# Optimization experiments

Hardware: AMD Instinct MI355X
Metric: run time of the kernel (lower is better)

Reference implementation:

```python
import jax, jax.numpy as jnp
import numpy as np

N_HEAD = 16
N_KV = 4
HEAD_DIM = 128
ROPE_BASE = 10000.0
YARN_ORIG = 2048
YARN_TARGET = 8192
YARN_ALPHA = 1.0
YARN_BETA = 1.0
SOFTCAP = 50.0


def _yarn_freqs(seq_len, start=0):
    # inv_freq with YaRN scaling: stretch by (target/orig)**alpha, magnitude 1/beta
    inv_freq = 1.0 / (ROPE_BASE ** (jnp.arange(0, HEAD_DIM, 2, dtype=jnp.float32) / HEAD_DIM))
    scale = (YARN_TARGET / YARN_ORIG) ** YARN_ALPHA
    inv_freq = inv_freq / scale * (1.0 / max(YARN_BETA, 1e-6))
    pos = jnp.arange(start, start + seq_len, dtype=jnp.float32)
    return pos[:, None] * inv_freq[None, :]  # [T, D/2]


def _apply_rope(x, freqs):
    # x: [B, H, T, D], interleaved even/odd rotation
    x_even = x[..., ::2]
    x_odd = x[..., 1::2]
    cos = jnp.cos(freqs)[None, None]  # [1,1,T,D/2]
    sin = jnp.sin(freqs)[None, None]
    y_even = x_even * cos - x_odd * sin
    y_odd = x_odd * cos + x_even * sin
    y = jnp.stack([y_even, y_odd], axis=-1).reshape(x.shape)
    return y


def setup_inputs() -> dict:
    key = jax.random.key(0)
    k1, k2, k3 = jax.random.split(key, 3)
    B, T, C = 2, 2048, 2048
    qkv_dim = (N_HEAD + 2 * N_KV) * HEAD_DIM  # 3072
    x = jax.random.normal(k1, (B, T, C), dtype=jnp.float32)
    w_qkv = jax.random.normal(k2, (C, qkv_dim), dtype=jnp.float32) * (1.0 / np.sqrt(C))
    w_o = jax.random.normal(k3, (C, C), dtype=jnp.float32) * (1.0 / np.sqrt(C))
    return {"x": x, "w_qkv": w_qkv, "w_o": w_o}


def reference(x, w_qkv, w_o):
    B, T, C = x.shape
    qkv = x @ w_qkv  # [B, T, (H+2*Hkv)*D]
    q_dim = N_HEAD * HEAD_DIM
    kv_dim = N_KV * HEAD_DIM
    q = qkv[..., :q_dim].reshape(B, T, N_HEAD, HEAD_DIM).transpose(0, 2, 1, 3)
    k = qkv[..., q_dim:q_dim + kv_dim].reshape(B, T, N_KV, HEAD_DIM).transpose(0, 2, 1, 3)
    v = qkv[..., q_dim + kv_dim:].reshape(B, T, N_KV, HEAD_DIM).transpose(0, 2, 1, 3)

    freqs = _yarn_freqs(T)
    q = _apply_rope(q, freqs)
    k = _apply_rope(k, freqs)

    # GQA: expand kv heads to query heads
    rep = N_HEAD // N_KV
    k = jnp.repeat(k, rep, axis=1)
    v = jnp.repeat(v, rep, axis=1)

    scores = jnp.einsum('bhqd,bhkd->bhqk', q, k) / jnp.sqrt(jnp.float32(HEAD_DIM))
    scores = SOFTCAP * jnp.tanh(scores / SOFTCAP)
    causal = jnp.tril(jnp.ones((T, T), dtype=bool))
    scores = jnp.where(causal[None, None], scores, jnp.float32(-1e9))
    attn = jax.nn.softmax(scores.astype(jnp.float32), axis=-1).astype(q.dtype)
    out = jnp.einsum('bhqk,bhkd->bhqd', attn, v)
    out = out.transpose(0, 2, 1, 3).reshape(B, T, C)
    return out @ w_o
```

## Files before the change

kernel.cpp:

```cpp
#include <hip/hip_runtime.h>
#include <hip/hip_bf16.h>

typedef __attribute__((ext_vector_type(8))) __bf16 bf16x8;
typedef __attribute__((ext_vector_type(2))) __bf16 bf16x2;
typedef __attribute__((ext_vector_type(4))) float f32x4;

#define T_SEQ 2048
#define C_DIM 2048
#define QKV_DIM 3072
#define NKV 4
#define HD 128

#define AS1 __attribute__((address_space(1)))
#define AS3 __attribute__((address_space(3)))

__device__ __forceinline__ unsigned short f2bf(float x) {
    __hip_bfloat16 h = __float2bfloat16(x);
    return __builtin_bit_cast(unsigned short, h);
}
__device__ __forceinline__ float bf2f(unsigned short u) {
    unsigned int i = ((unsigned int)u) << 16;
    return __builtin_bit_cast(float, i);
}
__device__ __forceinline__ unsigned int pkbf(float lo, float hi) {
#if __has_builtin(__builtin_amdgcn_cvt_pk_bf16_f32)
    bf16x2 r = __builtin_amdgcn_cvt_pk_bf16_f32(lo, hi);
    return __builtin_bit_cast(unsigned int, r);
#else
    return ((unsigned int)f2bf(hi) << 16) | (unsigned int)f2bf(lo);
#endif
}
__device__ __forceinline__ f32x4 mfma16(bf16x8 a, bf16x8 b, f32x4 c) {
    return __builtin_amdgcn_mfma_f32_16x16x32_bf16(a, b, c, 0, 0, 0);
}
__device__ __forceinline__ void gload_lds16(const void* g, void* l) {
    __builtin_amdgcn_global_load_lds((const AS1 unsigned int*)g,
                                     (AS3 unsigned int*)l, 16, 0, 0);
}
__device__ __forceinline__ float softcap_exp(float s) {
    const float CX2 = 3.125e-6f;
    const float CT  = 0.12752334197529714f;
    float x2 = s * s * CX2;
    float poly = fmaf(x2, fmaf(x2, 0.13333333f, -0.33333333f), 1.0f);
    return exp2f(s * CT * poly);
}

__global__ __launch_bounds__(256) void cast_f32_to_bf16(
        const float* __restrict__ in, unsigned short* __restrict__ out, int n4) {
    int i = blockIdx.x * 256 + threadIdx.x;
    if (i >= n4) return;
    float4 v = ((const float4*)in)[i];
    uint2 o;
    o.x = pkbf(v.x, v.y);
    o.y = pkbf(v.z, v.w);
    ((uint2*)out)[i] = o;
}

__global__ __launch_bounds__(256) void transpose_cast_f32_bf16(
        const float* __restrict__ in, unsigned short* __restrict__ out,
        int rows, int cols) {
    __shared__ float tile[32][33];
    int c0 = blockIdx.x * 32, r0 = blockIdx.y * 32;
    int tx = threadIdx.x, ty = threadIdx.y;
    #pragma unroll
    for (int i = 0; i < 4; i++)
        tile[ty + 8 * i][tx] = in[(size_t)(r0 + ty + 8 * i) * cols + c0 + tx];
    __syncthreads();
    #pragma unroll
    for (int i = 0; i < 4; i++)
        out[(size_t)(c0 + ty + 8 * i) * rows + r0 + tx] = f2bf(tile[tx][ty + 8 * i]);
}

__global__ __launch_bounds__(256) void pack_v(
        const unsigned short* __restrict__ qkv, unsigned short* __restrict__ vpack) {
    __shared__ unsigned short tile[32][33];
    int c0 = blockIdx.x * 32;
    int r0 = blockIdx.y * 32;
    int tx = threadIdx.x, ty = threadIdx.y;
    #pragma unroll
    for (int i = 0; i < 4; i++)
        tile[ty + 8 * i][tx] =
            qkv[(size_t)(r0 + ty + 8 * i) * QKV_DIM + 2560 + c0 + tx];
    __syncthreads();
    #pragma unroll
    for (int i = 0; i < 4; i++) {
        int dcol = c0 + ty + 8 * i;
        int kv = dcol >> 7, d = dcol & 127;
        int r = r0 + tx;
        int b = r >> 11, t = r & (T_SEQ - 1);
        vpack[(size_t)((b * NKV + kv) * 64 + (t >> 5)) * 4096 +
              (d >> 4) * 512 + ((t >> 3) & 3) * 128 + (d & 15) * 8 + (t & 7)] =
            tile[tx][ty + 8 * i];
    }
}

__global__ __launch_bounds__(256) void yarn_tab_kernel(float2* __restrict__ tab) {
    int idx = blockIdx.x * 256 + threadIdx.x;
    int t = idx >> 6, i = idx & 63;
    float inv = 0.25f * exp2f(-(float)i * (13.287712379549449f / 64.0f));
    float ang = (float)t * inv;
    float s, c;
    __sincosf(ang, &s, &c);
    tab[idx] = make_float2(c, s);
}

__global__ __launch_bounds__(256) void rope_kernel(
        unsigned short* __restrict__ qkv, const float2* __restrict__ tab,
        unsigned short* __restrict__ kpack) {
    int row = blockIdx.x;
    int t = row & (T_SEQ - 1);
    int b = row >> 11;
    const float2* tb = tab + t * 64;
    for (int p = threadIdx.x; p < 1280; p += 256) {
        int head = p >> 6, i = p & 63;
        float2 cs = tb[i];
        size_t idx = (size_t)row * QKV_DIM + head * 128 + 2 * i;
        unsigned int u = *(const unsigned int*)(qkv + idx);
        float e = bf2f((unsigned short)(u & 0xffff));
        float o = bf2f((unsigned short)(u >> 16));
        unsigned int res = pkbf(e * cs.x - o * cs.y, o * cs.x + e * cs.y);
        if (head < 16) {
            *(unsigned int*)(qkv + idx) = res;
        } else {
            int kvh = head - 16;
            unsigned short* dst = kpack +
                (size_t)((b * NKV + kvh) * 128 + (t >> 4)) * 2048 +
                (i >> 2) * 128 + (t & 15) * 8 + (i & 3) * 2;
            *(unsigned int*)dst = res;
        }
    }
}

template <int OUT_BF16>
__global__ __launch_bounds__(256) void gemm_bt(
        const unsigned short* __restrict__ A, const unsigned short* __restrict__ Bt,
        void* __restrict__ Cout, int M, int N, int K) {
    __shared__ __align__(16) unsigned short As[128 * 32];
    __shared__ __align__(16) unsigned short Bs[128 * 32];
    int tid = threadIdx.x;
    int nwg = gridDim.x * gridDim.y;
    int lid = blockIdx.y * gridDim.x + blockIdx.x;
    int work = (lid & 7) * (nwg >> 3) + (lid >> 3);
    int m0 = (work % gridDim.y) * 128;
    int n0 = (work / gridDim.y) * 128;
    int wave = tid >> 6, lane = tid & 63;
    int wm = (wave & 1) * 64, wn = (wave >> 1) * 64;
    int l15 = lane & 15, quad = lane >> 4;
    int lrow = lane >> 2, lcol = (lane & 3) * 8;

    f32x4 zf = {0.f, 0.f, 0.f, 0.f};
    f32x4 acc[4][4];
    #pragma unroll
    for (int i = 0; i < 4; i++)
        #pragma unroll
        for (int j = 0; j < 4; j++) acc[i][j] = zf;

    int ca = wave * 2;
    const unsigned short* gA = A + (size_t)(m0 + ca * 16 + lrow) * K + lcol;
    const unsigned short* gB = Bt + (size_t)(n0 + ca * 16 + lrow) * K + lcol;

    for (int k0 = 0; k0 < K; k0 += 32) {
        gload_lds16(gA + k0, &As[ca * 512]);
        gload_lds16(gA + k0 + 16 * (size_t)K, &As[ca * 512 + 512]);
        gload_lds16(gB + k0, &Bs[ca * 512]);
        gload_lds16(gB + k0 + 16 * (size_t)K, &Bs[ca * 512 + 512]);
        __syncthreads();
        bf16x8 af[4], bfr[4];
        #pragma unroll
        for (int i = 0; i < 4; i++)
            af[i] = *(const bf16x8*)&As[(wm + i * 16 + l15) * 32 + quad * 8];
        #pragma unroll
        for (int i = 0; i < 4; i++)
            bfr[i] = *(const bf16x8*)&Bs[(wn + i * 16 + l15) * 32 + quad * 8];
        #pragma unroll
        for (int mi = 0; mi < 4; mi++)
            #pragma unroll
            for (int ni = 0; ni < 4; ni++)
                acc[mi][ni] = mfma16(af[mi], bfr[ni], acc[mi][ni]);
        __syncthreads();
    }
    #pragma unroll
    for (int mi = 0; mi < 4; mi++)
        #pragma unroll
        for (int ni = 0; ni < 4; ni++) {
            int row = m0 + wm + mi * 16 + quad * 4;
            int col = n0 + wn + ni * 16 + l15;
            #pragma unroll
            for (int r = 0; r < 4; r++) {
                float v = acc[mi][ni][r];
                if (OUT_BF16)
                    ((unsigned short*)Cout)[(size_t)(row + r) * N + col] = f2bf(v);
                else
                    ((float*)Cout)[(size_t)(row + r) * N + col] = v;
            }
        }
}

__device__ __forceinline__ void attn_tile(
        const unsigned short* __restrict__ qkv,
        const unsigned short* __restrict__ kpack,
        const unsigned short* __restrict__ vpack,
        unsigned short* __restrict__ attn_out,
        unsigned int* __restrict__ pT, float* __restrict__ comb,
        int b, int hA, int qt, int wave, int lane) {
    int l15 = lane & 15, quad = lane >> 4;
    int kv = hA >> 2;
    f32x4 zf = {0.f, 0.f, 0.f, 0.f};

    const unsigned short* kb_ = kpack + ((size_t)(b * NKV + kv) * 128) * 2048 + lane * 8;
    const unsigned short* vb_ = vpack + ((size_t)(b * NKV + kv) * 64) * 4096 + lane * 8;

    int n = (qt >> 1) + 1;
    int half = n >> 1;
    int lo = wave ? half : 0;
    int hi = wave ? n : half;

    const unsigned short* qp =
        qkv + (size_t)(b * T_SEQ + qt * 16 + l15) * QKV_DIM + hA * HD + quad * 8;
    bf16x8 aqA[4], aqB[4];
    #pragma unroll
    for (int c = 0; c < 4; c++) {
        aqA[c] = *(const bf16x8*)(qp + c * 32);
        aqB[c] = *(const bf16x8*)(qp + HD + c * 32);
    }

    f32x4 oA[8], oB[8];
    #pragma unroll
    for (int d = 0; d < 8; d++) { oA[d] = zf; oB[d] = zf; }
    float lsA = 0.f, lsB = 0.f;
    int qglob = qt * 16 + l15;

    if (lo < hi) {
        bf16x8 KA[8], KB[8];
        auto loadK = [&](bf16x8* K, int t) {
            const unsigned short* a = kb_ + (size_t)t * 4096;
            #pragma unroll
            for (int c = 0; c < 4; c++) {
                K[c]     = *(const bf16x8*)(a + c * 512);
                K[4 + c] = *(const bf16x8*)(a + 2048 + c * 512);
            }
        };
        auto step = [&](const bf16x8* K, unsigned int* buf, int t,
                        bf16x8* Kpre, bool do_pre) {
            const unsigned short* v0 = vb_ + (size_t)t * 4096;
            bf16x8 Vv[8];
            #pragma unroll
            for (int dd = 0; dd < 8; dd++)
                Vv[dd] = *(const bf16x8*)(v0 + dd * 512);
            if (do_pre) loadK(Kpre, t + 1);
            f32x4 s0A = zf, s1A = zf, s0B = zf, s1B = zf;
            __builtin_amdgcn_s_setprio(1);
            #pragma unroll
            for (int c = 0; c < 4; c++) {
                s0A = mfma16(K[c],     aqA[c], s0A);
                s1A = mfma16(K[4 + c], aqA[c], s1A);
                s0B = mfma16(K[c],     aqB[c], s0B);
                s1B = mfma16(K[4 + c], aqB[c], s1B);
            }
            __builtin_amdgcn_s_setprio(0);
            bool masked = (t == n - 1);
            float p0A[4], p1A[4], p0B[4], p1B[4];
            int kb = t * 32 + quad * 4;
            #pragma unroll
            for (int r = 0; r < 4; r++) {
                float q0A = softcap_exp(s0A[r]);
                float q1A = softcap_exp(s1A[r]);
                float q0B = softcap_exp(s0B[r]);
                float q1B = softcap_exp(s1B[r]);
                if (masked) {
                    bool m0 = (kb + r <= qglob), m1 = (kb + 16 + r <= qglob);
                    q0A = m0 ? q0A : 0.f;  q1A = m1 ? q1A : 0.f;
                    q0B = m0 ? q0B : 0.f;  q1B = m1 ? q1B : 0.f;
                }
                p0A[r] = q0A; p1A[r] = q1A; lsA += q0A + q1A;
                p0B[r] = q0B; p1B[r] = q1B; lsB += q0B + q1B;
            }
            unsigned int* wpA = buf + l15 * 20 + quad * 2;
            unsigned int* wpB = wpA + 320;
            *(uint2*)wpA       = make_uint2(pkbf(p0A[0], p0A[1]), pkbf(p0A[2], p0A[3]));
            *(uint2*)(wpA + 8) = make_uint2(pkbf(p1A[0], p1A[1]), pkbf(p1A[2], p1A[3]));
            *(uint2*)wpB       = make_uint2(pkbf(p0B[0], p0B[1]), pkbf(p0B[2], p0B[3]));
            *(uint2*)(wpB + 8) = make_uint2(pkbf(p1B[0], p1B[1]), pkbf(p1B[2], p1B[3]));
            __asm__ volatile("s_waitcnt lgkmcnt(0)" ::: "memory");
            bf16x8 bpA = *(const bf16x8*)(buf + l15 * 20 + quad * 4);
            bf16x8 bpB = *(const bf16x8*)(buf + 320 + l15 * 20 + quad * 4);
            __builtin_amdgcn_s_setprio(1);
            #pragma unroll
            for (int dd = 0; dd < 8; dd++) {
                oA[dd] = mfma16(Vv[dd], bpA, oA[dd]);
                oB[dd] = mfma16(Vv[dd], bpB, oB[dd]);
            }
            __builtin_amdgcn_s_setprio(0);
        };

        loadK(KA, lo);
        int t = lo;
        while (true) {
            bool last = (t == hi - 1);
            step(KA, pT, t, KB, !last);
            if (last) break;
            t++;
            last = (t == hi - 1);
            step(KB, pT + 640, t, KA, !last);
            if (last) break;
            t++;
        }
    }

    float* slot = comb + lane * 34;
    if (wave == 0) {
        #pragma unroll
        for (int dd = 0; dd < 8; dd++)
            #pragma unroll
            for (int r = 0; r < 4; r++) slot[dd * 4 + r] = oB[dd][r];
        slot[32] = lsB;
    }
    __syncthreads();
    if (wave == 1) {
        #pragma unroll
        for (int dd = 0; dd < 8; dd++)
            #pragma unroll
            for (int r = 0; r < 4; r++) oB[dd][r] += slot[dd * 4 + r];
        lsB += slot[32];
        float l = lsB;
        l += __shfl_xor(l, 16);
        l += __shfl_xor(l, 32);
        float rl = __builtin_amdgcn_rcpf(l);
        unsigned short* op = attn_out +
            (size_t)(b * T_SEQ + qt * 16 + l15) * C_DIM + (hA + 1) * HD + quad * 4;
        #pragma unroll
        for (int dd = 0; dd < 8; dd++) {
            unsigned int u0 = pkbf(oB[dd][0] * rl, oB[dd][1] * rl);
            unsigned int u1 = pkbf(oB[dd][2] * rl, oB[dd][3] * rl);
            *(uint2*)(op + dd * 16) = make_uint2(u0, u1);
        }
    }
    __syncthreads();
    if (wave == 1) {
        #pragma unroll
        for (int dd = 0; dd < 8; dd++)
            #pragma unroll
            for (int r = 0; r < 4; r++) slot[dd * 4 + r] = oA[dd][r];
        slot[32] = lsA;
    }
    __syncthreads();
    if (wave == 0) {
        #pragma unroll
        for (int dd = 0; dd < 8; dd++)
            #pragma unroll
            for (int r = 0; r < 4; r++) oA[dd][r] += slot[dd * 4 + r];
        lsA += slot[32];
        float l = lsA;
        l += __shfl_xor(l, 16);
        l += __shfl_xor(l, 32);
        float rl = __builtin_amdgcn_rcpf(l);
        unsigned short* op = attn_out +
            (size_t)(b * T_SEQ + qt * 16 + l15) * C_DIM + hA * HD + quad * 4;
        #pragma unroll
        for (int dd = 0; dd < 8; dd++) {
            unsigned int u0 = pkbf(oA[dd][0] * rl, oA[dd][1] * rl);
            unsigned int u1 = pkbf(oA[dd][2] * rl, oA[dd][3] * rl);
            *(uint2*)(op + dd * 16) = make_uint2(u0, u1);
        }
    }
}

__global__ __launch_bounds__(128) void attn_kernel(
        const unsigned short* __restrict__ qkv,
        const unsigned short* __restrict__ kpack,
        const unsigned short* __restrict__ vpack,
        unsigned short* __restrict__ attn_out) {
    __shared__ __align__(16) unsigned int pT[2][1280];
    __shared__ float comb[64 * 34];
    int bid = blockIdx.x;
    int qt = 127 - (bid >> 4);
    int g = bid & 15;
    int b = g >> 3, pair = g & 7;
    int hA = pair * 2;
    int wave = threadIdx.x >> 6, lane = threadIdx.x & 63;
    attn_tile(qkv, kpack, vpack, attn_out, pT[wave], comb, b, hA, qt, wave, lane);
}

extern "C" void kernel_launch(void* const* d_in, const int* in_sizes, int n_in,
                              void* d_out, int out_size, void* d_ws, size_t ws_size,
                              hipStream_t stream) {
    (void)in_sizes; (void)n_in; (void)out_size; (void)ws_size;
    const float* x = (const float*)d_in[0];
    const float* w_qkv = (const float*)d_in[1];
    const float* w_o = (const float*)d_in[2];
    char* ws = (char*)d_ws;

    unsigned short* xbf   = (unsigned short*)(ws);
    unsigned short* wqkvT = (unsigned short*)(ws + 16777216);
    unsigned short* woT   = (unsigned short*)(ws + 29360128);
    unsigned short* qkv   = (unsigned short*)(ws + 37748736);
    unsigned short* kpack = (unsigned short*)(ws + 16777216);
    unsigned short* vpack = (unsigned short*)(ws + 20971520);
    float2*         tab   = (float2*)(ws + 62914560);
    unsigned short* attn  = xbf;

    cast_f32_to_bf16<<<8192, 256, 0, stream>>>(x, xbf, 2097152);
    transpose_cast_f32_bf16<<<dim3(96, 64), dim3(32, 8), 0, stream>>>(w_qkv, wqkvT, 2048, 3072);
    transpose_cast_f32_bf16<<<dim3(64, 64), dim3(32, 8), 0, stream>>>(w_o, woT, 2048, 2048);
    yarn_tab_kernel<<<512, 256, 0, stream>>>(tab);
    gemm_bt<1><<<dim3(24, 32), 256, 0, stream>>>(xbf, wqkvT, qkv, 4096, 3072, 2048);
    rope_kernel<<<4096, 256, 0, stream>>>(qkv, tab, kpack);
    pack_v<<<dim3(16, 128), dim3(32, 8), 0, stream>>>(qkv, vpack);
    attn_kernel<<<2048, 128, 0, stream>>>(qkv, kpack, vpack, attn);
    gemm_bt<0><<<dim3(16, 32), 256, 0, stream>>>(attn, woT, d_out, 4096, 2048, 2048);
}
```

Before: 343.0 us.

## Merge prep and rope/packv launches; deepen GEMM K-tile with swizzled LDS

Four preprocessing kernels (input cast, two weight transposes, YaRN table) become one launch that branches on block index, and rope plus V packing become a second merged launch. This removes several kernel-launch gaps. The bf16 GEMM now stages K=64 per iteration with an XOR-swizzled LDS layout, which halves the barriers per K step and is meant to avoid LDS bank conflicts on fragment reads. The cost is twice the LDS per block, which may lower occupancy.

```diff
diff --git a/kernel.cpp b/kernel.cpp
--- a/kernel.cpp
+++ b/kernel.cpp
@@ -45,88 +45,104 @@
     return exp2f(s * CT * poly);
 }
 
-__global__ __launch_bounds__(256) void cast_f32_to_bf16(
-        const float* __restrict__ in, unsigned short* __restrict__ out, int n4) {
-    int i = blockIdx.x * 256 + threadIdx.x;
-    if (i >= n4) return;
-    float4 v = ((const float4*)in)[i];
-    uint2 o;
-    o.x = pkbf(v.x, v.y);
-    o.y = pkbf(v.z, v.w);
-    ((uint2*)out)[i] = o;
-}
-
-__global__ __launch_bounds__(256) void transpose_cast_f32_bf16(
-        const float* __restrict__ in, unsigned short* __restrict__ out,
-        int rows, int cols) {
+__global__ __launch_bounds__(256) void prep_kernel(
+        const float* __restrict__ x, unsigned short* __restrict__ xbf,
+        const float* __restrict__ w_qkv, unsigned short* __restrict__ wqkvT,
+        const float* __restrict__ w_o, unsigned short* __restrict__ woT,
+        float2* __restrict__ tab) {
     __shared__ float tile[32][33];
-    int c0 = blockIdx.x * 32, r0 = blockIdx.y * 32;
-    int tx = threadIdx.x, ty = threadIdx.y;
-    #pragma unroll
-    for (int i = 0; i < 4; i++)
-        tile[ty + 8 * i][tx] = in[(size_t)(r0 + ty + 8 * i) * cols + c0 + tx];
-    __syncthreads();
-    #pragma unroll
-    for (int i = 0; i < 4; i++)
-        out[(size_t)(c0 + ty + 8 * i) * rows + r0 + tx] = f2bf(tile[tx][ty + 8 * i]);
-}
-
-__global__ __launch_bounds__(256) void pack_v(
-        const unsigned short* __restrict__ qkv, unsigned short* __restrict__ vpack) {
-    __shared__ unsigned short tile[32][33];
-    int c0 = blockIdx.x * 32;
-    int r0 = blockIdx.y * 32;
-    int tx = threadIdx.x, ty = threadIdx.y;
-    #pragma unroll
-    for (int i = 0; i < 4; i++)
-        tile[ty + 8 * i][tx] =
-            qkv[(size_t)(r0 + ty + 8 * i) * QKV_DIM + 2560 + c0 + tx];
-    __syncthreads();
-    #pragma unroll
-    for (int i = 0; i < 4; i++) {
-        int dcol = c0 + ty + 8 * i;
-        int kv = dcol >> 7, d = dcol & 127;
-        int r = r0 + tx;
-        int b = r >> 11, t = r & (T_SEQ - 1);
-        vpack[(size_t)((b * NKV + kv) * 64 + (t >> 5)) * 4096 +
-              (d >> 4) * 512 + ((t >> 3) & 3) * 128 + (d & 15) * 8 + (t & 7)] =
-            tile[tx][ty + 8 * i];
-    }
-}
-
-__global__ __launch_bounds__(256) void yarn_tab_kernel(float2* __restrict__ tab) {
-    int idx = blockIdx.x * 256 + threadIdx.x;
-    int t = idx >> 6, i = idx & 63;
-    float inv = 0.25f * exp2f(-(float)i * (13.287712379549449f / 64.0f));
-    float ang = (float)t * inv;
-    float s, c;
-    __sincosf(ang, &s, &c);
-    tab[idx] = make_float2(c, s);
-}
-
-__global__ __launch_bounds__(256) void rope_kernel(
+    int idx = blockIdx.x, tid = threadIdx.x;
+    if (idx < 8192) {
+        int i = idx * 256 + tid;
+        float4 v = ((const float4*)x)[i];
+        uint2 o;
+        o.x = pkbf(v.x, v.y);
+        o.y = pkbf(v.z, v.w);
+        ((uint2*)xbf)[i] = o;
+        return;
+    }
+    if (idx < 18432) {
+        const float* in;  unsigned short* out;  int rows, cols, bx, by;
+        if (idx < 14336) {
+            int pid = idx - 8192;
+            in = w_qkv; out = wqkvT; rows = 2048; cols = 3072;
+            bx = pid % 96; by = pid / 96;
+        } else {
+            int pid = idx - 14336;
+            in = w_o; out = woT; rows = 2048; cols = 2048;
+            bx = pid % 64; by = pid / 64;
+        }
+        int c0 = bx * 32, r0 = by * 32;
+        int tx = tid & 31, ty = tid >> 5;
+        #pragma unroll
+        for (int i = 0; i < 4; i++)
+            tile[ty + 8 * i][tx] = in[(size_t)(r0 + ty + 8 * i) * cols + c0 + tx];
+        __syncthreads();
+        #pragma unroll
+        for (int i = 0; i < 4; i++)
+            out[(size_t)(c0 + ty + 8 * i) * rows + r0 + tx] = f2bf(tile[tx][ty + 8 * i]);
+        return;
+    }
+    {
+        int i2 = (idx - 18432) * 256 + tid;
+        int t = i2 >> 6, i = i2 & 63;
+        float inv = 0.25f * exp2f(-(float)i * (13.287712379549449f / 64.0f));
+        float ang = (float)t * inv;
+        float s, c;
+        __sincosf(ang, &s, &c);
+        tab[i2] = make_float2(c, s);
+    }
+}
+
+__global__ __launch_bounds__(256) void rope_packv_kernel(
         unsigned short* __restrict__ qkv, const float2* __restrict__ tab,
-        unsigned short* __restrict__ kpack) {
-    int row = blockIdx.x;
-    int t = row & (T_SEQ - 1);
-    int b = row >> 11;
-    const float2* tb = tab + t * 64;
-    for (int p = threadIdx.x; p < 1280; p += 256) {
-        int head = p >> 6, i = p & 63;
-        float2 cs = tb[i];
-        size_t idx = (size_t)row * QKV_DIM + head * 128 + 2 * i;
-        unsigned int u = *(const unsigned int*)(qkv + idx);
-        float e = bf2f((unsigned short)(u & 0xffff));
-        float o = bf2f((unsigned short)(u >> 16));
-        unsigned int res = pkbf(e * cs.x - o * cs.y, o * cs.x + e * cs.y);
-        if (head < 16) {
-            *(unsigned int*)(qkv + idx) = res;
-        } else {
-            int kvh = head - 16;
-            unsigned short* dst = kpack +
-                (size_t)((b * NKV + kvh) * 128 + (t >> 4)) * 2048 +
-                (i >> 2) * 128 + (t & 15) * 8 + (i & 3) * 2;
-            *(unsigned int*)dst = res;
+        unsigned short* __restrict__ kpack, unsigned short* __restrict__ vpack) {
+    __shared__ unsigned short stile[32][33];
+    int idx = blockIdx.x, tid = threadIdx.x;
+    if (idx < 4096) {
+        int row = idx;
+        int t = row & (T_SEQ - 1);
+        int b = row >> 11;
+        const float2* tb = tab + t * 64;
+        for (int p = tid; p < 1280; p += 256) {
+            int head = p >> 6, i = p & 63;
+            float2 cs = tb[i];
+            size_t qidx = (size_t)row * QKV_DIM + head * 128 + 2 * i;
+            unsigned int u = *(const unsigned int*)(qkv + qidx);
+            float e = bf2f((unsigned short)(u & 0xffff));
+            float o = bf2f((unsigned short)(u >> 16));
+            unsigned int res = pkbf(e * cs.x - o * cs.y, o * cs.x + e * cs.y);
+            if (head < 16) {
+                *(unsigned int*)(qkv + qidx) = res;
+            } else {
+                int kvh = head - 16;
+                unsigned short* dst = kpack +
+                    (size_t)((b * NKV + kvh) * 128 + (t >> 4)) * 2048 +
+                    (i >> 2) * 128 + (t & 15) * 8 + (i & 3) * 2;
+                *(unsigned int*)dst = res;
+            }
+        }
+        return;
+    }
+    {
+        int pid = idx - 4096;
+        int c0 = (pid & 15) * 32;
+        int r0 = (pid >> 4) * 32;
+        int tx = tid & 31, ty = tid >> 5;
+        #pragma unroll
+        for (int i = 0; i < 4; i++)
+            stile[ty + 8 * i][tx] =
+                qkv[(size_t)(r0 + ty + 8 * i) * QKV_DIM + 2560 + c0 + tx];
+        __syncthreads();
+        #pragma unroll
+        for (int i = 0; i < 4; i++) {
+            int dcol = c0 + ty + 8 * i;
+            int kv = dcol >> 7, d = dcol & 127;
+            int r = r0 + tx;
+            int b = r >> 11, t = r & (T_SEQ - 1);
+            vpack[(size_t)((b * NKV + kv) * 64 + (t >> 5)) * 4096 +
+                  (d >> 4) * 512 + ((t >> 3) & 3) * 128 + (d & 15) * 8 + (t & 7)] =
+                stile[tx][ty + 8 * i];
         }
     }
 }
@@ -135,8 +151,8 @@
 __global__ __launch_bounds__(256) void gemm_bt(
         const unsigned short* __restrict__ A, const unsigned short* __restrict__ Bt,
         void* __restrict__ Cout, int M, int N, int K) {
-    __shared__ __align__(16) unsigned short As[128 * 32];
-    __shared__ __align__(16) unsigned short Bs[128 * 32];
+    __shared__ __align__(16) unsigned short As[128 * 64];
+    __shared__ __align__(16) unsigned short Bs[128 * 64];
     int tid = threadIdx.x;
     int nwg = gridDim.x * gridDim.y;
     int lid = blockIdx.y * gridDim.x + blockIdx.x;
@@ -146,7 +162,8 @@
     int wave = tid >> 6, lane = tid & 63;
     int wm = (wave & 1) * 64, wn = (wave >> 1) * 64;
     int l15 = lane & 15, quad = lane >> 4;
-    int lrow = lane >> 2, lcol = (lane & 3) * 8;
+    int lrow8 = lane >> 3;
+    int swz8 = (lane & 7) ^ lrow8;
 
     f32x4 zf = {0.f, 0.f, 0.f, 0.f};
     f32x4 acc[4][4];
@@ -155,28 +172,36 @@
         #pragma unroll
         for (int j = 0; j < 4; j++) acc[i][j] = zf;
 
-    int ca = wave * 2;
-    const unsigned short* gA = A + (size_t)(m0 + ca * 16 + lrow) * K + lcol;
-    const unsigned short* gB = Bt + (size_t)(n0 + ca * 16 + lrow) * K + lcol;
-
-    for (int k0 = 0; k0 < K; k0 += 32) {
-        gload_lds16(gA + k0, &As[ca * 512]);
-        gload_lds16(gA + k0 + 16 * (size_t)K, &As[ca * 512 + 512]);
-        gload_lds16(gB + k0, &Bs[ca * 512]);
-        gload_lds16(gB + k0 + 16 * (size_t)K, &Bs[ca * 512 + 512]);
+    const unsigned short* gA = A + (size_t)(m0 + wave * 32 + lrow8) * K + swz8 * 8;
+    const unsigned short* gB = Bt + (size_t)(n0 + wave * 32 + lrow8) * K + swz8 * 8;
+    unsigned short* lA = &As[(wave * 4) * 512];
+    unsigned short* lB = &Bs[(wave * 4) * 512];
+    int rsw = (l15 & 7) << 3;
+
+    for (int k0 = 0; k0 < K; k0 += 64) {
+        #pragma unroll
+        for (int l = 0; l < 4; l++) {
+            gload_lds16(gA + k0 + (size_t)l * 8 * K, lA + l * 512);
+            gload_lds16(gB + k0 + (size_t)l * 8 * K, lB + l * 512);
+        }
         __syncthreads();
-        bf16x8 af[4], bfr[4];
-        #pragma unroll
-        for (int i = 0; i < 4; i++)
-            af[i] = *(const bf16x8*)&As[(wm + i * 16 + l15) * 32 + quad * 8];
-        #pragma unroll
-        for (int i = 0; i < 4; i++)
-            bfr[i] = *(const bf16x8*)&Bs[(wn + i * 16 + l15) * 32 + quad * 8];
-        #pragma unroll
-        for (int mi = 0; mi < 4; mi++)
-            #pragma unroll
-            for (int ni = 0; ni < 4; ni++)
-                acc[mi][ni] = mfma16(af[mi], bfr[ni], acc[mi][ni]);
+        #pragma unroll
+        for (int kk = 0; kk < 2; kk++) {
+            bf16x8 af[4], bfr[4];
+            #pragma unroll
+            for (int i = 0; i < 4; i++)
+                af[i] = *(const bf16x8*)&As[(wm + i * 16 + l15) * 64 +
+                                            (((kk * 4 + quad) << 3) ^ rsw)];
+            #pragma unroll
+            for (int i = 0; i < 4; i++)
+                bfr[i] = *(const bf16x8*)&Bs[(wn + i * 16 + l15) * 64 +
+                                             (((kk * 4 + quad) << 3) ^ rsw)];
+            #pragma unroll
+            for (int mi = 0; mi < 4; mi++)
+                #pragma unroll
+                for (int ni = 0; ni < 4; ni++)
+                    acc[mi][ni] = mfma16(af[mi], bfr[ni], acc[mi][ni]);
+        }
         __syncthreads();
     }
     #pragma unroll
@@ -399,13 +424,9 @@
     float2*         tab   = (float2*)(ws + 62914560);
     unsigned short* attn  = xbf;
 
-    cast_f32_to_bf16<<<8192, 256, 0, stream>>>(x, xbf, 2097152);
-    transpose_cast_f32_bf16<<<dim3(96, 64), dim3(32, 8), 0, stream>>>(w_qkv, wqkvT, 2048, 3072);
-    transpose_cast_f32_bf16<<<dim3(64, 64), dim3(32, 8), 0, stream>>>(w_o, woT, 2048, 2048);
-    yarn_tab_kernel<<<512, 256, 0, stream>>>(tab);
+    prep_kernel<<<18944, 256, 0, stream>>>(x, xbf, w_qkv, wqkvT, w_o, woT, tab);
     gemm_bt<1><<<dim3(24, 32), 256, 0, stream>>>(xbf, wqkvT, qkv, 4096, 3072, 2048);
-    rope_kernel<<<4096, 256, 0, stream>>>(qkv, tab, kpack);
-    pack_v<<<dim3(16, 128), dim3(32, 8), 0, stream>>>(qkv, vpack);
+    rope_packv_kernel<<<6144, 256, 0, stream>>>(qkv, tab, kpack, vpack);
     attn_kernel<<<2048, 128, 0, stream>>>(qkv, kpack, vpack, attn);
     gemm_bt<0><<<dim3(16, 32), 256, 0, stream>>>(attn, woT, d_out, 4096, 2048, 2048);
 }
```

Measured after the change: 329.5 us. -3.9%, faster.
